# Performance work log

Hardware: AMD Instinct MI355X
Metric: run time of the kernel (lower is better)

## Reference

```python
import jax, jax.numpy as jnp
import numpy as np

N, NN, S = 128, 16, 64        # agents, neighbors, timesteps
D, DK, DV, H, DFF = 128, 32, 32, 4, 512


def _ln(x, g, b, eps=1e-5):
    m = x.mean(-1, keepdims=True)
    v = ((x - m) ** 2).mean(-1, keepdims=True)
    return (x - m) / jnp.sqrt(v + eps) * g + b


def setup_inputs() -> dict:
    key = jax.random.key(0)
    ks = jax.random.split(key, 12)
    s = 0.02
    return {
        "x_emb": jax.random.normal(ks[0], (N, S, D), jnp.float32),
        "neighbor_emb": jax.random.normal(ks[1], (N, NN, S, D), jnp.float32),
        "attn_mask": jax.random.randint(ks[2], (N, NN, S, S), 0, 2) > 0,
        "att_factor": jnp.float32(1.0),
        "W_Q": jax.random.normal(ks[3], (D, H * DK), jnp.float32) * s,
        "W_K": jax.random.normal(ks[4], (D, H * DK), jnp.float32) * s,
        "W_V": jax.random.normal(ks[5], (D, H * DV), jnp.float32) * s,
        "W_fc": jax.random.normal(ks[6], (H * DV, D), jnp.float32) * s,
        "ln_mha_g": jnp.ones((D,), jnp.float32),
        "ln_mha_b": jnp.zeros((D,), jnp.float32),
        "W_SI": jax.random.normal(ks[7], (H * D, D), jnp.float32) * s,
        "W1_self": jax.random.normal(ks[8], (D, DFF), jnp.float32) * s,
        "W2_self": jax.random.normal(ks[9], (DFF, D), jnp.float32) * s,
        "ln_self_g": jnp.ones((D,), jnp.float32),
        "ln_self_b": jnp.zeros((D,), jnp.float32),
        "W1_inter": jax.random.normal(ks[10], (D, DFF), jnp.float32) * s,
        "W2_inter": jax.random.normal(ks[11], (DFF, D), jnp.float32) * s,
        "ln_inter_g": jnp.ones((D,), jnp.float32),
        "ln_inter_b": jnp.zeros((D,), jnp.float32),
    }


def reference(x_emb, neighbor_emb, attn_mask, att_factor,
              W_Q, W_K, W_V, W_fc, ln_mha_g, ln_mha_b,
              W_SI, W1_self, W2_self, ln_self_g, ln_self_b,
              W1_inter, W2_inter, ln_inter_g, ln_inter_b):
    n, nn, s, d = neighbor_emb.shape
    # --- MHA over neighbor embeddings (masked softmax attention) ---
    Q = (neighbor_emb @ W_Q).reshape(n, nn, s, H, DK).transpose(0, 1, 3, 2, 4)
    K = (neighbor_emb @ W_K).reshape(n, nn, s, H, DK).transpose(0, 1, 3, 2, 4)
    V = (neighbor_emb @ W_V).reshape(n, nn, s, H, DV).transpose(0, 1, 3, 2, 4)
    scores = jnp.einsum('bnhsd,bnhtd->bnhst', Q, K) / np.sqrt(DK)
    scores = jnp.where(attn_mask[:, :, None, :, :], scores, jnp.float32(-1e9))
    attn_inter = jax.nn.softmax(scores, axis=-1)          # (N,NN,H,S,S)
    res = jnp.einsum('bnhst,bnhtd->bnhsd', attn_inter, V)
    res = res.transpose(0, 1, 3, 2, 4).reshape(n, nn, s, H * DV)
    res_inter = _ln(res @ W_fc + neighbor_emb, ln_mha_g, ln_mha_b)
    # --- self attention map on x_emb (no projections) ---
    att_i = attn_inter.mean(1)                            # mean over neighbors -> (N,H,S,S)
    scores_self = jnp.einsum('bsd,btd->bst', x_emb, x_emb) / np.sqrt(d)
    att_self = jax.nn.softmax(scores_self, axis=-1)       # (N,S,S)
    att = att_self[:, None, :, :] + att_factor * att_i    # (N,H,S,S)
    # --- apply fused attention to x_emb ---
    res_si = jnp.einsum('bhst,btd->bhsd', att, x_emb)     # (N,H,S,D)
    x = res_si.transpose(0, 2, 1, 3).reshape(n, s, H * d)
    x = x @ W_SI
    x = _ln(jnp.maximum(x @ W1_self, 0.0) @ W2_self + x, ln_self_g, ln_self_b)
    nb = _ln(jnp.maximum(res_inter @ W1_inter, 0.0) @ W2_inter + res_inter,
             ln_inter_g, ln_inter_b)
    return (x, nb)
```

## Files before the change

kernel.cpp:

```cpp
#include <hip/hip_runtime.h>
#include <hip/hip_bf16.h>

#define NA   128
#define NN_  16
#define SS   64
#define DD   128
#define HH   4

typedef __attribute__((ext_vector_type(8))) short bf16x8;
typedef __attribute__((ext_vector_type(4))) float floatx4;
typedef __attribute__((ext_vector_type(4))) short shortx4;

#define MFMA16(a, b, c) __builtin_amdgcn_mfma_f32_16x16x32_bf16((a), (b), (c), 0, 0, 0)

__device__ __forceinline__ short F2BS(float f) {
    __hip_bfloat16 h = __float2bfloat16(f);
    short s;
    __builtin_memcpy(&s, &h, 2);
    return s;
}

__device__ __forceinline__ int swz(int row, int col, int ld) {
    const int byte = ((row * ld + col) << 1) ^ ((row & 7) << 4);
    return byte >> 1;
}

__global__ __launch_bounds__(256) void k_prep(
    const float* __restrict__ Wq, const float* __restrict__ Wk,
    const float* __restrict__ Wv,
    const float* __restrict__ Wfc, const float* __restrict__ W1i,
    const float* __restrict__ W2i, const float* __restrict__ WSI,
    const float* __restrict__ W1s, const float* __restrict__ W2s,
    short* __restrict__ WqT, short* __restrict__ WkT, short* __restrict__ WvT,
    short* __restrict__ WfcT, short* __restrict__ W1iT, short* __restrict__ W2iT,
    short* __restrict__ WSIT, short* __restrict__ W1sT, short* __restrict__ W2sT)
{
    const int i = blockIdx.x * 256 + threadIdx.x;
    if (i < 128 * 128) {
        const int n = i >> 7, k = i & 127;
        const int src = k * 128 + n;
        WqT[i]  = F2BS(Wq[src]);
        WkT[i]  = F2BS(Wk[src]);
        WvT[i]  = F2BS(Wv[src]);
        WfcT[i] = F2BS(Wfc[src]);
    }
    {
        const int n = i >> 7, k = i & 127;
        W1iT[i] = F2BS(W1i[k * 512 + n]);
        W1sT[i] = F2BS(W1s[k * 512 + n]);
    }
    {
        const int n = i >> 9, f = i & 511;
        W2iT[i] = F2BS(W2i[f * 128 + n]);
        W2sT[i] = F2BS(W2s[f * 128 + n]);
        WSIT[i] = F2BS(WSI[f * 128 + n]);
    }
}

__global__ __launch_bounds__(256) void k_attn(
    const float* __restrict__ nbr,
    const int* __restrict__ mask,
    const short* __restrict__ WqT,
    const short* __restrict__ WkT,
    const short* __restrict__ WvT,
    float* __restrict__ att_sum,
    float* __restrict__ res_ws)
{
    const int bn  = blockIdx.x;
    const int b   = bn >> 4;
    const int tid = threadIdx.x;
    const int lane = tid & 63, quad = lane >> 4, l16 = lane & 15;
    const int m0 = (tid >> 6) * 16;

    __shared__ short shE[64 * 128];
    __shared__ short shQ[64 * 128];
    __shared__ short shK[64 * 128];
    __shared__ short shVT[128 * 64];
    short* const shP = shE;

    const float* E = nbr + (size_t)bn * 8192;
    for (int i = tid; i < 2048; i += 256) {
        const floatx4 v = *(const floatx4*)&E[i * 4];
        const int row = i >> 5, col = (i & 31) * 4;
        shortx4 o;
#pragma unroll
        for (int j = 0; j < 4; ++j) o[j] = F2BS(v[j]);
        *(shortx4*)&shE[swz(row, col, 128)] = o;
    }

    const int* mrow = mask + (size_t)bn * 4096;
    int mv[4][4];
#pragma unroll
    for (int nt = 0; nt < 4; ++nt)
#pragma unroll
        for (int r = 0; r < 4; ++r)
            mv[nt][r] = mrow[(m0 + quad * 4 + r) * 64 + nt * 16 + l16];

    __syncthreads();

    bf16x8 ax[4];
#pragma unroll
    for (int kt = 0; kt < 4; ++kt)
        ax[kt] = *(const bf16x8*)&shE[swz(m0 + l16, kt * 32 + quad * 8, 128)];

#pragma unroll
    for (int nt = 0; nt < 8; ++nt) {
        floatx4 aq = {0.f, 0.f, 0.f, 0.f};
        floatx4 ak = {0.f, 0.f, 0.f, 0.f};
        floatx4 av = {0.f, 0.f, 0.f, 0.f};
#pragma unroll
        for (int kt = 0; kt < 4; ++kt) {
            const size_t wo = (size_t)(nt * 16 + l16) * 128 + kt * 32 + quad * 8;
            aq = MFMA16(ax[kt], *(const bf16x8*)&WqT[wo], aq);
            ak = MFMA16(ax[kt], *(const bf16x8*)&WkT[wo], ak);
            av = MFMA16(ax[kt], *(const bf16x8*)&WvT[wo], av);
        }
        shortx4 ov;
#pragma unroll
        for (int r = 0; r < 4; ++r) {
            const int row = m0 + quad * 4 + r, col = nt * 16 + l16;
            shQ[swz(row, col, 128)] = F2BS(aq[r]);
            shK[swz(row, col, 128)] = F2BS(ak[r]);
            ov[r] = F2BS(av[r]);
        }
        *(shortx4*)&shVT[swz(nt * 16 + l16, m0 + quad * 4, 64)] = ov;
    }
    __syncthreads();

    const float iscale = 0.17677669529663687f;
    float* const out = res_ws + (size_t)bn * 8192;

    for (int h = 0; h < 4; ++h) {
        const bf16x8 qa = *(const bf16x8*)&shQ[swz(m0 + l16, h * 32 + quad * 8, 128)];
        floatx4 sa[4];
#pragma unroll
        for (int nt = 0; nt < 4; ++nt) {
            const bf16x8 kb = *(const bf16x8*)&shK[swz(nt * 16 + l16, h * 32 + quad * 8, 128)];
            const floatx4 z = {0.f, 0.f, 0.f, 0.f};
            sa[nt] = MFMA16(qa, kb, z);
        }
        float p[4][4];
#pragma unroll
        for (int r = 0; r < 4; ++r) {
            float m = -1e30f;
#pragma unroll
            for (int nt = 0; nt < 4; ++nt) {
                p[nt][r] = mv[nt][r] ? sa[nt][r] * iscale : -1e9f;
                m = fmaxf(m, p[nt][r]);
            }
            m = fmaxf(m, __shfl_xor(m, 1, 64));
            m = fmaxf(m, __shfl_xor(m, 2, 64));
            m = fmaxf(m, __shfl_xor(m, 4, 64));
            m = fmaxf(m, __shfl_xor(m, 8, 64));
            float sum = 0.f;
#pragma unroll
            for (int nt = 0; nt < 4; ++nt) {
                const float e = __expf(p[nt][r] - m);
                p[nt][r] = e; sum += e;
            }
            sum += __shfl_xor(sum, 1, 64);
            sum += __shfl_xor(sum, 2, 64);
            sum += __shfl_xor(sum, 4, 64);
            sum += __shfl_xor(sum, 8, 64);
            const float inv = 1.f / sum;
#pragma unroll
            for (int nt = 0; nt < 4; ++nt) p[nt][r] *= inv;
        }
        float* const as = att_sum + ((size_t)(b * 4 + h)) * 4096;
#pragma unroll
        for (int nt = 0; nt < 4; ++nt)
#pragma unroll
            for (int r = 0; r < 4; ++r) {
                const int row = m0 + quad * 4 + r, col = nt * 16 + l16;
                atomicAdd(as + row * 64 + col, p[nt][r]);
                shP[swz(row, col, 64)] = F2BS(p[nt][r]);
            }
        const bf16x8 pa0 = *(const bf16x8*)&shP[swz(m0 + l16, quad * 8, 64)];
        const bf16x8 pa1 = *(const bf16x8*)&shP[swz(m0 + l16, 32 + quad * 8, 64)];
#pragma unroll
        for (int nt = 0; nt < 2; ++nt) {
            floatx4 acc = {0.f, 0.f, 0.f, 0.f};
            acc = MFMA16(pa0, *(const bf16x8*)&shVT[swz(h * 32 + nt * 16 + l16, quad * 8, 64)], acc);
            acc = MFMA16(pa1, *(const bf16x8*)&shVT[swz(h * 32 + nt * 16 + l16, 32 + quad * 8, 64)], acc);
#pragma unroll
            for (int r = 0; r < 4; ++r)
                out[(m0 + quad * 4 + r) * 128 + h * 32 + nt * 16 + l16] = acc[r];
        }
    }
}

__device__ __forceinline__ void ffn_mfma(
    const short* shA, short* shH, floatx4 (&accO)[8],
    const short* __restrict__ W1T,
    const short* __restrict__ W2T,
    const float* __restrict__ g, const float* __restrict__ bb,
    float* outp, int m0, int lane)
{
    const int quad = lane >> 4, l16 = lane & 15;

    bf16x8 ax[4];
#pragma unroll
    for (int kt = 0; kt < 4; ++kt)
        ax[kt] = *(const bf16x8*)&shA[swz(m0 + l16, kt * 32 + quad * 8, 128)];

#pragma unroll
    for (int fc = 0; fc < 4; ++fc) {
#pragma unroll
        for (int nt = 0; nt < 8; ++nt) {
            floatx4 acc = {0.f, 0.f, 0.f, 0.f};
            const int n0 = fc * 128 + nt * 16;
#pragma unroll
            for (int kt = 0; kt < 4; ++kt) {
                bf16x8 bf = *(const bf16x8*)&W1T[(size_t)(n0 + l16) * 128 + kt * 32 + quad * 8];
                acc = MFMA16(ax[kt], bf, acc);
            }
#pragma unroll
            for (int r = 0; r < 4; ++r)
                shH[swz(m0 + quad * 4 + r, nt * 16 + l16, 128)] = F2BS(fmaxf(acc[r], 0.f));
        }
        bf16x8 ah[4];
#pragma unroll
        for (int kt = 0; kt < 4; ++kt)
            ah[kt] = *(const bf16x8*)&shH[swz(m0 + l16, kt * 32 + quad * 8, 128)];
#pragma unroll
        for (int nt = 0; nt < 8; ++nt)
#pragma unroll
            for (int kt = 0; kt < 4; ++kt) {
                bf16x8 bf = *(const bf16x8*)&W2T[(size_t)(nt * 16 + l16) * 512 + fc * 128 + kt * 32 + quad * 8];
                accO[nt] = MFMA16(ah[kt], bf, accO[nt]);
            }
    }

    float mean[4], rstd[4];
#pragma unroll
    for (int r = 0; r < 4; ++r) {
        float p = 0.f;
#pragma unroll
        for (int nt = 0; nt < 8; ++nt) p += accO[nt][r];
        p += __shfl_xor(p, 1, 64); p += __shfl_xor(p, 2, 64);
        p += __shfl_xor(p, 4, 64); p += __shfl_xor(p, 8, 64);
        mean[r] = p * (1.f / 128.f);
        float q = 0.f;
#pragma unroll
        for (int nt = 0; nt < 8; ++nt) { const float d = accO[nt][r] - mean[r]; q += d * d; }
        q += __shfl_xor(q, 1, 64); q += __shfl_xor(q, 2, 64);
        q += __shfl_xor(q, 4, 64); q += __shfl_xor(q, 8, 64);
        rstd[r] = rsqrtf(q * (1.f / 128.f) + 1e-5f);
    }
#pragma unroll
    for (int nt = 0; nt < 8; ++nt) {
        const int colc = nt * 16 + l16;
        const float gc = g[colc], bc = bb[colc];
#pragma unroll
        for (int r = 0; r < 4; ++r) {
            const int row = m0 + quad * 4 + r;
            outp[row * 128 + colc] = (accO[nt][r] - mean[r]) * rstd[r] * gc + bc;
        }
    }
}

__device__ __forceinline__ void ln_inplace(
    floatx4 (&acc)[8], const float* __restrict__ g, const float* __restrict__ bb,
    short* shX, int m0, int quad, int l16)
{
    float mean[4], rstd[4];
#pragma unroll
    for (int r = 0; r < 4; ++r) {
        float p = 0.f;
#pragma unroll
        for (int nt = 0; nt < 8; ++nt) p += acc[nt][r];
        p += __shfl_xor(p, 1, 64); p += __shfl_xor(p, 2, 64);
        p += __shfl_xor(p, 4, 64); p += __shfl_xor(p, 8, 64);
        mean[r] = p * (1.f / 128.f);
        float q = 0.f;
#pragma unroll
        for (int nt = 0; nt < 8; ++nt) { const float d = acc[nt][r] - mean[r]; q += d * d; }
        q += __shfl_xor(q, 1, 64); q += __shfl_xor(q, 2, 64);
        q += __shfl_xor(q, 4, 64); q += __shfl_xor(q, 8, 64);
        rstd[r] = rsqrtf(q * (1.f / 128.f) + 1e-5f);
    }
#pragma unroll
    for (int nt = 0; nt < 8; ++nt) {
        const int colc = nt * 16 + l16;
        const float gc = g[colc], bc = bb[colc];
#pragma unroll
        for (int r = 0; r < 4; ++r) {
            acc[nt][r] = (acc[nt][r] - mean[r]) * rstd[r] * gc + bc;
            shX[swz(m0 + quad * 4 + r, colc, 128)] = F2BS(acc[nt][r]);
        }
    }
}

__global__ __launch_bounds__(256, 2) void k_mha_ffn(
    const float* __restrict__ nbr,
    const float* res_in,
    const short* __restrict__ WfcT,
    const float* __restrict__ g1, const float* __restrict__ b1,
    const short* __restrict__ W1T, const short* __restrict__ W2T,
    const float* __restrict__ g2, const float* __restrict__ b2,
    float* out_nb)
{
    const int bn0 = blockIdx.x * 2;
    const int tid = threadIdx.x;
    const int lane = tid & 63, quad = lane >> 4, l16 = lane & 15;
    const int m0 = (tid >> 6) * 16;
    __shared__ short lds0[64 * 128];
    __shared__ short lds1[64 * 128];

    const float* rp0 = res_in + (size_t)bn0 * 8192;
    const float* rp1 = res_in + (size_t)(bn0 + 1) * 8192;
    for (int j = lane; j < 512; j += 64) {
        const int row = m0 + (j >> 5), col = (j & 31) * 4;
        const floatx4 v0 = *(const floatx4*)&rp0[row * 128 + col];
        const floatx4 v1 = *(const floatx4*)&rp1[row * 128 + col];
        shortx4 o0, o1;
#pragma unroll
        for (int t = 0; t < 4; ++t) { o0[t] = F2BS(v0[t]); o1[t] = F2BS(v1[t]); }
        *(shortx4*)&lds0[swz(row, col, 128)] = o0;
        *(shortx4*)&lds1[swz(row, col, 128)] = o1;
    }

    bf16x8 ax0[4], ax1[4];
#pragma unroll
    for (int kt = 0; kt < 4; ++kt) {
        ax0[kt] = *(const bf16x8*)&lds0[swz(m0 + l16, kt * 32 + quad * 8, 128)];
        ax1[kt] = *(const bf16x8*)&lds1[swz(m0 + l16, kt * 32 + quad * 8, 128)];
    }

    floatx4 acc0[8], acc1[8];
    const float* E0 = nbr + (size_t)bn0 * 8192;
    const float* E1 = nbr + (size_t)(bn0 + 1) * 8192;
#pragma unroll
    for (int nt = 0; nt < 8; ++nt)
#pragma unroll
        for (int r = 0; r < 4; ++r) {
            const int idx = (m0 + quad * 4 + r) * 128 + nt * 16 + l16;
            acc0[nt][r] = E0[idx];
            acc1[nt][r] = E1[idx];
        }
#pragma unroll
    for (int nt = 0; nt < 8; ++nt)
#pragma unroll
        for (int kt = 0; kt < 4; ++kt) {
            bf16x8 bf = *(const bf16x8*)&WfcT[(size_t)(nt * 16 + l16) * 128 + kt * 32 + quad * 8];
            acc0[nt] = MFMA16(ax0[kt], bf, acc0[nt]);
            acc1[nt] = MFMA16(ax1[kt], bf, acc1[nt]);
        }

    ln_inplace(acc0, g1, b1, lds0, m0, quad, l16);
    ln_inplace(acc1, g1, b1, lds1, m0, quad, l16);

#pragma unroll
    for (int kt = 0; kt < 4; ++kt) {
        ax0[kt] = *(const bf16x8*)&lds0[swz(m0 + l16, kt * 32 + quad * 8, 128)];
        ax1[kt] = *(const bf16x8*)&lds1[swz(m0 + l16, kt * 32 + quad * 8, 128)];
    }

#pragma unroll
    for (int fc = 0; fc < 4; ++fc) {
#pragma unroll
        for (int nt = 0; nt < 8; ++nt) {
            floatx4 h0 = {0.f, 0.f, 0.f, 0.f};
            floatx4 h1 = {0.f, 0.f, 0.f, 0.f};
            const int n0 = fc * 128 + nt * 16;
#pragma unroll
            for (int kt = 0; kt < 4; ++kt) {
                bf16x8 bf = *(const bf16x8*)&W1T[(size_t)(n0 + l16) * 128 + kt * 32 + quad * 8];
                h0 = MFMA16(ax0[kt], bf, h0);
                h1 = MFMA16(ax1[kt], bf, h1);
            }
#pragma unroll
            for (int r = 0; r < 4; ++r) {
                const int o = swz(m0 + quad * 4 + r, nt * 16 + l16, 128);
                lds0[o] = F2BS(fmaxf(h0[r], 0.f));
                lds1[o] = F2BS(fmaxf(h1[r], 0.f));
            }
        }
        bf16x8 ah0[4], ah1[4];
#pragma unroll
        for (int kt = 0; kt < 4; ++kt) {
            ah0[kt] = *(const bf16x8*)&lds0[swz(m0 + l16, kt * 32 + quad * 8, 128)];
            ah1[kt] = *(const bf16x8*)&lds1[swz(m0 + l16, kt * 32 + quad * 8, 128)];
        }
#pragma unroll
        for (int nt = 0; nt < 8; ++nt)
#pragma unroll
            for (int kt = 0; kt < 4; ++kt) {
                bf16x8 bf = *(const bf16x8*)&W2T[(size_t)(nt * 16 + l16) * 512 + fc * 128 + kt * 32 + quad * 8];
                acc0[nt] = MFMA16(ah0[kt], bf, acc0[nt]);
                acc1[nt] = MFMA16(ah1[kt], bf, acc1[nt]);
            }
    }

    float* const op0 = out_nb + (size_t)bn0 * 8192;
    float* const op1 = out_nb + (size_t)(bn0 + 1) * 8192;
    {
        float mean[4], rstd[4];
#pragma unroll
        for (int r = 0; r < 4; ++r) {
            float p = 0.f;
#pragma unroll
            for (int nt = 0; nt < 8; ++nt) p += acc0[nt][r];
            p += __shfl_xor(p, 1, 64); p += __shfl_xor(p, 2, 64);
            p += __shfl_xor(p, 4, 64); p += __shfl_xor(p, 8, 64);
            mean[r] = p * (1.f / 128.f);
            float q = 0.f;
#pragma unroll
            for (int nt = 0; nt < 8; ++nt) { const float d = acc0[nt][r] - mean[r]; q += d * d; }
            q += __shfl_xor(q, 1, 64); q += __shfl_xor(q, 2, 64);
            q += __shfl_xor(q, 4, 64); q += __shfl_xor(q, 8, 64);
            rstd[r] = rsqrtf(q * (1.f / 128.f) + 1e-5f);
        }
#pragma unroll
        for (int nt = 0; nt < 8; ++nt) {
            const int colc = nt * 16 + l16;
            const float gc = g2[colc], bc = b2[colc];
#pragma unroll
            for (int r = 0; r < 4; ++r)
                op0[(m0 + quad * 4 + r) * 128 + colc] = (acc0[nt][r] - mean[r]) * rstd[r] * gc + bc;
        }
    }
    {
        float mean[4], rstd[4];
#pragma unroll
        for (int r = 0; r < 4; ++r) {
            float p = 0.f;
#pragma unroll
            for (int nt = 0; nt < 8; ++nt) p += acc1[nt][r];
            p += __shfl_xor(p, 1, 64); p += __shfl_xor(p, 2, 64);
            p += __shfl_xor(p, 4, 64); p += __shfl_xor(p, 8, 64);
            mean[r] = p * (1.f / 128.f);
            float q = 0.f;
#pragma unroll
            for (int nt = 0; nt < 8; ++nt) { const float d = acc1[nt][r] - mean[r]; q += d * d; }
            q += __shfl_xor(q, 1, 64); q += __shfl_xor(q, 2, 64);
            q += __shfl_xor(q, 4, 64); q += __shfl_xor(q, 8, 64);
            rstd[r] = rsqrtf(q * (1.f / 128.f) + 1e-5f);
        }
#pragma unroll
        for (int nt = 0; nt < 8; ++nt) {
            const int colc = nt * 16 + l16;
            const float gc = g2[colc], bc = b2[colc];
#pragma unroll
            for (int r = 0; r < 4; ++r)
                op1[(m0 + quad * 4 + r) * 128 + colc] = (acc1[nt][r] - mean[r]) * rstd[r] * gc + bc;
        }
    }
}

__global__ __launch_bounds__(256) void k_self(
    const float* __restrict__ xemb,
    const float* __restrict__ att_sum,
    const float* __restrict__ attf,
    float* __restrict__ res_si)
{
    const int bh = blockIdx.x;
    const int b = bh >> 2;
    const int tid = threadIdx.x;
    __shared__ float xe[64 * 129];
    __shared__ float A[64 * 65];

    const float* xp = xemb + (size_t)b * 8192;
    for (int i = tid; i < 8192; i += 256) xe[(i >> 7) * 129 + (i & 127)] = xp[i];
    __syncthreads();

    const float isc = 0.08838834764831845f;
    for (int i = tid; i < 4096; i += 256) {
        const int s = i >> 6, t = i & 63;
        const float* xs = xe + s * 129;
        const float* xt = xe + t * 129;
        float a0 = 0.f, a1 = 0.f, a2 = 0.f, a3 = 0.f;
#pragma unroll
        for (int d = 0; d < 128; d += 4) {
            a0 += xs[d]     * xt[d];
            a1 += xs[d + 1] * xt[d + 1];
            a2 += xs[d + 2] * xt[d + 2];
            a3 += xs[d + 3] * xt[d + 3];
        }
        A[s * 65 + t] = ((a0 + a1) + (a2 + a3)) * isc;
    }
    __syncthreads();
    if (tid < 64) {
        float* r = A + tid * 65;
        float m = r[0];
        for (int t = 1; t < 64; ++t) m = fmaxf(m, r[t]);
        float sum = 0.f;
        for (int t = 0; t < 64; ++t) { const float e = __expf(r[t] - m); r[t] = e; sum += e; }
        const float inv = 1.f / sum;
        for (int t = 0; t < 64; ++t) r[t] *= inv;
    }
    __syncthreads();
    const float f = attf[0] * (1.f / 16.f);
    const float* as = att_sum + (size_t)bh * 4096;
    for (int i = tid; i < 4096; i += 256)
        A[(i >> 6) * 65 + (i & 63)] += f * as[i];
    __syncthreads();

    float* op = res_si + (size_t)bh * 8192;
    for (int i = tid; i < 8192; i += 256) {
        const int s = i >> 7, d = i & 127;
        const float* ar = A + s * 65;
        float a0 = 0.f, a1 = 0.f;
#pragma unroll
        for (int t = 0; t < 64; t += 2) {
            a0 += ar[t]     * xe[t * 129 + d];
            a1 += ar[t + 1] * xe[(t + 1) * 129 + d];
        }
        op[i] = a0 + a1;
    }
}

__global__ __launch_bounds__(256, 2) void k_si_ffn(
    const float* __restrict__ res_si,
    const short* __restrict__ WSIT,
    const short* __restrict__ W1T, const short* __restrict__ W2T,
    const float* __restrict__ g, const float* __restrict__ bb,
    float* __restrict__ out_x)
{
    const int b = blockIdx.x, tid = threadIdx.x;
    const int w = tid >> 6, lane = tid & 63, quad = lane >> 4, l16 = lane & 15;
    const int m0 = w * 16;
    __shared__ short shC[64 * 512];
    short* shA = shC;
    short* shH = shC + 64 * 128;

    const float* rs = res_si + (size_t)b * 4 * 8192;
    for (int i = lane; i < 8192; i += 64) {
        const int row = m0 + (i >> 9), k = i & 511;
        const int h = k >> 7, d = k & 127;
        shC[swz(row, k, 512)] = F2BS(rs[((size_t)h * 64 + row) * 128 + d]);
    }

    floatx4 acc1[8];
#pragma unroll
    for (int nt = 0; nt < 8; ++nt) acc1[nt] = (floatx4){0.f, 0.f, 0.f, 0.f};
    for (int kt = 0; kt < 16; ++kt) {
        bf16x8 a = *(const bf16x8*)&shC[swz(m0 + l16, kt * 32 + quad * 8, 512)];
#pragma unroll
        for (int nt = 0; nt < 8; ++nt) {
            bf16x8 bf = *(const bf16x8*)&WSIT[(size_t)(nt * 16 + l16) * 512 + kt * 32 + quad * 8];
            acc1[nt] = MFMA16(a, bf, acc1[nt]);
        }
    }

    __syncthreads();

#pragma unroll
    for (int nt = 0; nt < 8; ++nt)
#pragma unroll
        for (int r = 0; r < 4; ++r)
            shA[swz(m0 + quad * 4 + r, nt * 16 + l16, 128)] = F2BS(acc1[nt][r]);

    ffn_mfma(shA, shH, acc1, W1T, W2T, g, bb, out_x + (size_t)b * 8192, m0, lane);
}

extern "C" void kernel_launch(void* const* d_in, const int* in_sizes, int n_in,
                              void* d_out, int out_size, void* d_ws, size_t ws_size,
                              hipStream_t stream) {
    const float* x_emb = (const float*)d_in[0];
    const float* nbr   = (const float*)d_in[1];
    const int*   mask  = (const int*)d_in[2];
    const float* attf  = (const float*)d_in[3];
    const float* Wq    = (const float*)d_in[4];
    const float* Wk    = (const float*)d_in[5];
    const float* Wv    = (const float*)d_in[6];
    const float* Wfc   = (const float*)d_in[7];
    const float* g_mha = (const float*)d_in[8];
    const float* b_mha = (const float*)d_in[9];
    const float* WSI   = (const float*)d_in[10];
    const float* W1s   = (const float*)d_in[11];
    const float* W2s   = (const float*)d_in[12];
    const float* gs    = (const float*)d_in[13];
    const float* bs    = (const float*)d_in[14];
    const float* W1i   = (const float*)d_in[15];
    const float* W2i   = (const float*)d_in[16];
    const float* gi    = (const float*)d_in[17];
    const float* bi    = (const float*)d_in[18];

    float* att_sum = (float*)d_ws;
    float* res_si = (float*)((char*)d_ws + (size_t)8 * 1024 * 1024 + 256);
    short* wqkv = (short*)((char*)d_ws + (size_t)25 * 1024 * 1024);
    short* WqT  = wqkv;
    short* WkT  = WqT + 16384;
    short* WvT  = WkT + 16384;
    short* wb   = (short*)((char*)d_ws + (size_t)26 * 1024 * 1024);
    short* WfcT = wb;
    short* W1iT = WfcT + 16384;
    short* W2iT = W1iT + 65536;
    short* WSIT = W2iT + 65536;
    short* W1sT = WSIT + 65536;
    short* W2sT = W1sT + 65536;

    float* out_x  = (float*)d_out;
    float* out_nb = out_x + (size_t)NA * SS * DD;
    float* res_ws = out_nb;

    hipMemsetAsync(d_ws, 0, (size_t)NA * HH * SS * SS * sizeof(float), stream);

    k_prep<<<256, 256, 0, stream>>>(Wq, Wk, Wv, Wfc, W1i, W2i, WSI, W1s, W2s,
                                    WqT, WkT, WvT,
                                    WfcT, W1iT, W2iT, WSIT, W1sT, W2sT);
    k_attn<<<NA * NN_, 256, 0, stream>>>(nbr, mask, WqT, WkT, WvT,
                                         att_sum, res_ws);
    k_mha_ffn<<<NA * NN_ / 2, 256, 0, stream>>>(nbr, res_ws, WfcT, g_mha, b_mha,
                                                W1iT, W2iT, gi, bi, out_nb);
    k_self<<<NA * HH, 256, 0, stream>>>(x_emb, att_sum, attf, res_si);
    k_si_ffn<<<NA, 256, 0, stream>>>(res_si, WSIT, W1sT, W2sT, gs, bs, out_x);
}
```

Baseline: 627.9 us.

## Replace attention-map atomics with bf16 per-neighbor stores reduced in k_self

Instead of every neighbor block atomically adding its softmax probabilities into a shared per-agent fp32 buffer, k_attn writes bf16 probabilities per (agent, neighbor, head) to a workspace. k_self then sums the 16 neighbor maps itself, and the memset is skipped. This removes heavy atomic contention and the zeroing pass, at the cost of about 64 MB of extra global writes and reads and bf16 rounding in the averaged map. The path is used only when the workspace is large enough, otherwise it falls back to the atomics.

```diff
diff --git a/kernel.cpp b/kernel.cpp
--- a/kernel.cpp
+++ b/kernel.cpp
@@ -18,6 +18,13 @@
     short s;
     __builtin_memcpy(&s, &h, 2);
     return s;
+}
+
+__device__ __forceinline__ float BS2F(short s) {
+    unsigned u = ((unsigned)(unsigned short)s) << 16;
+    float f;
+    __builtin_memcpy(&f, &u, 4);
+    return f;
 }
 
 __device__ __forceinline__ int swz(int row, int col, int ld) {
@@ -64,6 +71,7 @@
     const short* __restrict__ WkT,
     const short* __restrict__ WvT,
     float* __restrict__ att_sum,
+    short* __restrict__ P_ws,
     float* __restrict__ res_ws)
 {
     const int bn  = blockIdx.x;
@@ -166,15 +174,28 @@
 #pragma unroll
             for (int nt = 0; nt < 4; ++nt) p[nt][r] *= inv;
         }
-        float* const as = att_sum + ((size_t)(b * 4 + h)) * 4096;
-#pragma unroll
-        for (int nt = 0; nt < 4; ++nt)
-#pragma unroll
-            for (int r = 0; r < 4; ++r) {
-                const int row = m0 + quad * 4 + r, col = nt * 16 + l16;
-                atomicAdd(as + row * 64 + col, p[nt][r]);
-                shP[swz(row, col, 64)] = F2BS(p[nt][r]);
-            }
+        if (P_ws) {
+            short* const pp = P_ws + ((size_t)(bn * 4 + h)) * 4096;
+#pragma unroll
+            for (int nt = 0; nt < 4; ++nt)
+#pragma unroll
+                for (int r = 0; r < 4; ++r) {
+                    const int row = m0 + quad * 4 + r, col = nt * 16 + l16;
+                    const short v = F2BS(p[nt][r]);
+                    pp[row * 64 + col] = v;
+                    shP[swz(row, col, 64)] = v;
+                }
+        } else {
+            float* const as = att_sum + ((size_t)(b * 4 + h)) * 4096;
+#pragma unroll
+            for (int nt = 0; nt < 4; ++nt)
+#pragma unroll
+                for (int r = 0; r < 4; ++r) {
+                    const int row = m0 + quad * 4 + r, col = nt * 16 + l16;
+                    atomicAdd(as + row * 64 + col, p[nt][r]);
+                    shP[swz(row, col, 64)] = F2BS(p[nt][r]);
+                }
+        }
         const bf16x8 pa0 = *(const bf16x8*)&shP[swz(m0 + l16, quad * 8, 64)];
         const bf16x8 pa1 = *(const bf16x8*)&shP[swz(m0 + l16, 32 + quad * 8, 64)];
 #pragma unroll
@@ -451,11 +472,13 @@
 __global__ __launch_bounds__(256) void k_self(
     const float* __restrict__ xemb,
     const float* __restrict__ att_sum,
+    const short* __restrict__ P_ws,
     const float* __restrict__ attf,
     float* __restrict__ res_si)
 {
     const int bh = blockIdx.x;
     const int b = bh >> 2;
+    const int h = bh & 3;
     const int tid = threadIdx.x;
     __shared__ float xe[64 * 129];
     __shared__ float A[64 * 65];
@@ -491,9 +514,20 @@
     }
     __syncthreads();
     const float f = attf[0] * (1.f / 16.f);
-    const float* as = att_sum + (size_t)bh * 4096;
-    for (int i = tid; i < 4096; i += 256)
-        A[(i >> 6) * 65 + (i & 63)] += f * as[i];
+    if (P_ws) {
+        const short* pb = P_ws + ((size_t)(b * 16) * 4 + h) * 4096;
+        for (int i = tid; i < 4096; i += 256) {
+            float s = 0.f;
+#pragma unroll
+            for (int nn = 0; nn < 16; ++nn)
+                s += BS2F(pb[(size_t)nn * 4 * 4096 + i]);
+            A[(i >> 6) * 65 + (i & 63)] += f * s;
+        }
+    } else {
+        const float* as = att_sum + (size_t)bh * 4096;
+        for (int i = tid; i < 4096; i += 256)
+            A[(i >> 6) * 65 + (i & 63)] += f * as[i];
+    }
     __syncthreads();
 
     float* op = res_si + (size_t)bh * 8192;
@@ -578,8 +612,8 @@
     const float* bi    = (const float*)d_in[18];
 
     float* att_sum = (float*)d_ws;
-    float* res_si = (float*)((char*)d_ws + (size_t)8 * 1024 * 1024 + 256);
-    short* wqkv = (short*)((char*)d_ws + (size_t)25 * 1024 * 1024);
+    float* res_si = (float*)((char*)d_ws + (size_t)8 * 1024 * 1024 + 512 * 1024);
+    short* wqkv = (short*)((char*)d_ws + (size_t)25 * 1024 * 1024 + 512 * 1024);
     short* WqT  = wqkv;
     short* WkT  = WqT + 16384;
     short* WvT  = WkT + 16384;
@@ -591,19 +625,26 @@
     short* W1sT = WSIT + 65536;
     short* W2sT = W1sT + 65536;
 
+    const size_t pws_off  = (size_t)27 * 1024 * 1024;
+    const size_t pws_size = (size_t)NA * NN_ * HH * SS * SS * sizeof(short);
+    short* P_ws = nullptr;
+    if (ws_size >= pws_off + pws_size)
+        P_ws = (short*)((char*)d_ws + pws_off);
+
     float* out_x  = (float*)d_out;
     float* out_nb = out_x + (size_t)NA * SS * DD;
     float* res_ws = out_nb;
 
-    hipMemsetAsync(d_ws, 0, (size_t)NA * HH * SS * SS * sizeof(float), stream);
+    if (!P_ws)
+        hipMemsetAsync(d_ws, 0, (size_t)NA * HH * SS * SS * sizeof(float), stream);
 
     k_prep<<<256, 256, 0, stream>>>(Wq, Wk, Wv, Wfc, W1i, W2i, WSI, W1s, W2s,
                                     WqT, WkT, WvT,
                                     WfcT, W1iT, W2iT, WSIT, W1sT, W2sT);
     k_attn<<<NA * NN_, 256, 0, stream>>>(nbr, mask, WqT, WkT, WvT,
-                                         att_sum, res_ws);
+                                         att_sum, P_ws, res_ws);
     k_mha_ffn<<<NA * NN_ / 2, 256, 0, stream>>>(nbr, res_ws, WfcT, g_mha, b_mha,
                                                 W1iT, W2iT, gi, bi, out_nb);
-    k_self<<<NA * HH, 256, 0, stream>>>(x_emb, att_sum, attf, res_si);
+    k_self<<<NA * HH, 256, 0, stream>>>(x_emb, att_sum, P_ws, attf, res_si);
     k_si_ffn<<<NA, 256, 0, stream>>>(res_si, WSIT, W1sT, W2sT, gs, bs, out_x);
 }
```

New measurement: 601.4 us. 4.2% less time.
